# Performance work log

Measured on AMD Instinct MI355X. Metric: run time of the kernel, lower is better.

The kernel has to match this reference:

```python
import jax, jax.numpy as jnp
import numpy as np

H = 32          # hidden_size
L = 10          # linear_size
EPS = 1e-14


def _lstm_cell(x, h, c, Wih, Whh, bih, bhh):
    # torch LSTMCell: gates ordered [i, f, g, o]
    gates = x @ Wih.T + bih + h @ Whh.T + bhh
    i, f, g, o = jnp.split(gates, 4, axis=-1)
    i = jax.nn.sigmoid(i)
    f = jax.nn.sigmoid(f)
    g = jnp.tanh(g)
    o = jax.nn.sigmoid(o)
    c_new = f * c + i * g
    h_new = o * jnp.tanh(c_new)
    return h_new, c_new


def setup_inputs() -> dict:
    key = jax.random.key(0)
    ks = jax.random.split(key, 24)
    B, N = 8, 100000
    inp = {
        "x": jax.random.normal(ks[0], (B, N), jnp.float32),
        "grad": jax.random.normal(ks[1], (B, N), jnp.float32),
        "h0": jax.random.normal(ks[2], (B, N, H), jnp.float32),
        "c0": jax.random.normal(ks[3], (B, N, H), jnp.float32),
        "h1": jax.random.normal(ks[4], (B, N, H), jnp.float32),
        "c1": jax.random.normal(ks[5], (B, N, H), jnp.float32),
        # initial_transform: Linear(2, L) -> tanh -> Linear(L, L)
        "W1": jax.random.normal(ks[6], (L, 2), jnp.float32) * 0.3,
        "b1": jax.random.normal(ks[7], (L,), jnp.float32) * 0.1,
        "W2": jax.random.normal(ks[8], (L, L), jnp.float32) * 0.3,
        "b2": jax.random.normal(ks[9], (L,), jnp.float32) * 0.1,
        # LSTMCell layer 0 (input L) and layer 1 (input H)
        "Wih0": jax.random.normal(ks[10], (4 * H, L), jnp.float32) * 0.1,
        "Whh0": jax.random.normal(ks[11], (4 * H, H), jnp.float32) * 0.1,
        "bih0": jax.random.normal(ks[12], (4 * H,), jnp.float32) * 0.1,
        "bhh0": jax.random.normal(ks[13], (4 * H,), jnp.float32) * 0.1,
        "Wih1": jax.random.normal(ks[14], (4 * H, H), jnp.float32) * 0.1,
        "Whh1": jax.random.normal(ks[15], (4 * H, H), jnp.float32) * 0.1,
        "bih1": jax.random.normal(ks[16], (4 * H,), jnp.float32) * 0.1,
        "bhh1": jax.random.normal(ks[17], (4 * H,), jnp.float32) * 0.1,
        # fc: Linear(H, 1)
        "Wfc": jax.random.normal(ks[18], (1, H), jnp.float32) * 0.1,
        "bfc": jax.random.normal(ks[19], (1,), jnp.float32) * 0.1,
    }
    return inp


def reference(x, grad, h0, c0, h1, c1, W1, b1, W2, b2,
              Wih0, Whh0, bih0, bhh0, Wih1, Whh1, bih1, bhh1, Wfc, bfc):
    B, N = x.shape
    BN = B * N
    g = grad.reshape(BN, 1)
    # gradient preprocessing: [sign, log(|g| + eps)]
    inp = jnp.concatenate([jnp.sign(g), jnp.log(jnp.abs(g) + EPS)], axis=1)  # (BN, 2)
    t = jnp.tanh(inp @ W1.T + b1) @ W2.T + b2                                # (BN, L)
    # batched across all n variables simultaneously (no cross-variable recurrence)
    h0n, c0n = _lstm_cell(t, h0.reshape(BN, H), c0.reshape(BN, H), Wih0, Whh0, bih0, bhh0)
    h1n, c1n = _lstm_cell(h0n, h1.reshape(BN, H), c1.reshape(BN, H), Wih1, Whh1, bih1, bhh1)
    delta = (h1n @ Wfc.T + bfc).reshape(B, N)
    x_new = x + delta
    return (x_new,
            h0n.reshape(B, N, H), c0n.reshape(B, N, H),
            h1n.reshape(B, N, H), c1n.reshape(B, N, H),
            delta)
```

## Files before the change

kernel.cpp:

```cpp
#include <hip/hip_runtime.h>


typedef __attribute__((ext_vector_type(8))) short bf16x8;
typedef __attribute__((ext_vector_type(4))) float f32x4;

#define HH 32
#define LL 10
#define NG 128
#define NW 8
#define BLK 512

__device__ __forceinline__ short f2bf(float x) {
  __bf16 b = (__bf16)x;
  return __builtin_bit_cast(short, b);
}
__device__ __forceinline__ float fsig(float x) {
  return __builtin_amdgcn_rcpf(1.0f + __expf(-x));
}
__device__ __forceinline__ float ftanh(float x) {
  return fmaf(2.0f, __builtin_amdgcn_rcpf(1.0f + __expf(-2.0f * x)), -1.0f);
}

__global__ __launch_bounds__(BLK, 2) void l2o_fused(
    const float* __restrict__ x, const float* __restrict__ grad,
    const float* __restrict__ h0, const float* __restrict__ c0,
    const float* __restrict__ h1, const float* __restrict__ c1,
    const float* __restrict__ W1, const float* __restrict__ b1,
    const float* __restrict__ W2, const float* __restrict__ b2,
    const float* __restrict__ Wih0, const float* __restrict__ Whh0,
    const float* __restrict__ bih0, const float* __restrict__ bhh0,
    const float* __restrict__ Wih1, const float* __restrict__ Whh1,
    const float* __restrict__ bih1, const float* __restrict__ bhh1,
    const float* __restrict__ Wfc, const float* __restrict__ bfc,
    float* __restrict__ out, int BNi)
{
  const size_t BN = (size_t)BNi;
  float* __restrict__ xout  = out;
  float* __restrict__ h0out = out + BN;
  float* __restrict__ c0out = out + BN + BN * HH;
  float* __restrict__ h1out = out + BN + 2 * BN * HH;
  float* __restrict__ c1out = out + BN + 3 * BN * HH;
  float* __restrict__ dout  = out + BN + 4 * BN * HH;

  __shared__ __align__(16) short wih0L[2][NG][8];
  __shared__ __align__(16) short whh0L[4][NG][8];
  __shared__ __align__(16) short wih1L[4][NG][8];
  __shared__ __align__(16) short whh1L[4][NG][8];
  __shared__ __align__(16) short tsg0[NW][64][8];
  __shared__ __align__(4)  short tsg1[NW][64][2];
  __shared__ __align__(16) short hsg[NW][4][16][8];

  const int tid = threadIdx.x;
  for (int idx = tid; idx < NG * HH; idx += BLK) {
    int n = idx >> 5, k = idx & 31;
    whh0L[k >> 3][n][k & 7] = f2bf(Whh0[n * HH + k]);
    wih1L[k >> 3][n][k & 7] = f2bf(Wih1[n * HH + k]);
    whh1L[k >> 3][n][k & 7] = f2bf(Whh1[n * HH + k]);
  }
  for (int idx = tid; idx < NG * 16; idx += BLK) {
    int n = idx >> 4, k = idx & 15;
    wih0L[k >> 3][n][k & 7] = (k < LL) ? f2bf(Wih0[n * LL + k]) : (short)0;
  }

  const int lane = tid & 63;
  const int w = tid >> 6;
  const int col = lane & 15;
  const int g = lane >> 4;
  const int mrow = 4 * g;

  float biasv0[8], biasv1[8];
#pragma unroll
  for (int nt = 0; nt < 8; ++nt) {
    biasv0[nt] = bih0[nt * 16 + col] + bhh0[nt * 16 + col];
    biasv1[nt] = bih1[nt * 16 + col] + bhh1[nt * 16 + col];
  }
  const float wfc0 = Wfc[col], wfc1 = Wfc[16 + col];
  const float bfcv = bfc[0];

  const int ebase = blockIdx.x * (NW * 64) + w * 64;
  const bool active = ebase < BNi;

  if (active) {
    float gv = grad[ebase + lane];
    float sg = (gv > 0.f) ? 1.f : ((gv < 0.f) ? -1.f : 0.f);
    float lg = __logf(fabsf(gv) + 1e-14f);
    float u[LL], t[LL];
#pragma unroll
    for (int j = 0; j < LL; ++j)
      u[j] = ftanh(W1[2 * j] * sg + W1[2 * j + 1] * lg + b1[j]);
#pragma unroll
    for (int j = 0; j < LL; ++j) {
      float a = b2[j];
#pragma unroll
      for (int k = 0; k < LL; ++k) a += W2[j * LL + k] * u[k];
      t[j] = a;
    }
    bf16x8 tv0;
#pragma unroll
    for (int s = 0; s < 8; ++s) tv0[s] = f2bf(t[s]);
    *reinterpret_cast<bf16x8*>(&tsg0[w][lane][0]) = tv0;
    tsg1[w][lane][0] = f2bf(t[8]);
    tsg1[w][lane][1] = f2bf(t[9]);
  }
  __syncthreads();

  if (active) {
#pragma unroll 1
  for (int st = 0; st < 4; ++st) {
    const int m16 = ebase + st * 16;

    bf16x8 a_t = {0, 0, 0, 0, 0, 0, 0, 0};
    if (g == 0) a_t = *reinterpret_cast<const bf16x8*>(&tsg0[w][st * 16 + col][0]);
    else if (g == 1) {
      a_t[0] = tsg1[w][st * 16 + col][0];
      a_t[1] = tsg1[w][st * 16 + col][1];
    }
    const float4* hp = reinterpret_cast<const float4*>(h0 + (size_t)(m16 + col) * HH + 8 * g);
    float4 v0 = hp[0], v1 = hp[1];
    bf16x8 a_h0;
    a_h0[0] = f2bf(v0.x); a_h0[1] = f2bf(v0.y); a_h0[2] = f2bf(v0.z); a_h0[3] = f2bf(v0.w);
    a_h0[4] = f2bf(v1.x); a_h0[5] = f2bf(v1.y); a_h0[6] = f2bf(v1.z); a_h0[7] = f2bf(v1.w);

    float c0r[2][4];
#pragma unroll
    for (int kk = 0; kk < 2; ++kk)
#pragma unroll
      for (int r = 0; r < 4; ++r)
        c0r[kk][r] = c0[(size_t)(m16 + mrow + r) * HH + kk * 16 + col];

    f32x4 acc[8];
#pragma unroll
    for (int nt = 0; nt < 8; ++nt) {
      float bv = biasv0[nt];
      f32x4 a = {bv, bv, bv, bv};
      acc[nt] = a;
    }
#pragma unroll
    for (int nt = 0; nt < 8; ++nt) {
      bf16x8 bih = {0, 0, 0, 0, 0, 0, 0, 0};
      if (g < 2) bih = *reinterpret_cast<const bf16x8*>(&wih0L[g][nt * 16 + col][0]);
      acc[nt] = __builtin_amdgcn_mfma_f32_16x16x32_bf16(a_t, bih, acc[nt], 0, 0, 0);
      bf16x8 bhh = *reinterpret_cast<const bf16x8*>(&whh0L[g][nt * 16 + col][0]);
      acc[nt] = __builtin_amdgcn_mfma_f32_16x16x32_bf16(a_h0, bhh, acc[nt], 0, 0, 0);
    }

    const float4* h1p = reinterpret_cast<const float4*>(h1 + (size_t)(m16 + col) * HH + 8 * g);
    float4 w0 = h1p[0], w1v = h1p[1];

#pragma unroll
    for (int kk = 0; kk < 2; ++kk) {
      const int k = kk * 16 + col;
#pragma unroll
      for (int r = 0; r < 4; ++r) {
        const size_t e2 = (size_t)(m16 + mrow + r);
        float iv = fsig(acc[0 + kk][r]);
        float fv = fsig(acc[2 + kk][r]);
        float gv = ftanh(acc[4 + kk][r]);
        float ov = fsig(acc[6 + kk][r]);
        float cn = fv * c0r[kk][r] + iv * gv;
        float hn = ov * ftanh(cn);
        c0out[e2 * HH + k] = cn;
        h0out[e2 * HH + k] = hn;
        hsg[w][k >> 3][mrow + r][k & 7] = f2bf(hn);
      }
    }
    asm volatile("s_waitcnt lgkmcnt(0)" ::: "memory");

    bf16x8 a_hn = *reinterpret_cast<const bf16x8*>(&hsg[w][g][col][0]);
    bf16x8 a_h1;
    a_h1[0] = f2bf(w0.x);  a_h1[1] = f2bf(w0.y);  a_h1[2] = f2bf(w0.z);  a_h1[3] = f2bf(w0.w);
    a_h1[4] = f2bf(w1v.x); a_h1[5] = f2bf(w1v.y); a_h1[6] = f2bf(w1v.z); a_h1[7] = f2bf(w1v.w);

    float c1r[2][4];
#pragma unroll
    for (int kk = 0; kk < 2; ++kk)
#pragma unroll
      for (int r = 0; r < 4; ++r)
        c1r[kk][r] = c1[(size_t)(m16 + mrow + r) * HH + kk * 16 + col];

#pragma unroll
    for (int nt = 0; nt < 8; ++nt) {
      float bv = biasv1[nt];
      f32x4 a = {bv, bv, bv, bv};
      acc[nt] = a;
    }
#pragma unroll
    for (int nt = 0; nt < 8; ++nt) {
      bf16x8 bih = *reinterpret_cast<const bf16x8*>(&wih1L[g][nt * 16 + col][0]);
      acc[nt] = __builtin_amdgcn_mfma_f32_16x16x32_bf16(a_hn, bih, acc[nt], 0, 0, 0);
      bf16x8 bhh = *reinterpret_cast<const bf16x8*>(&whh1L[g][nt * 16 + col][0]);
      acc[nt] = __builtin_amdgcn_mfma_f32_16x16x32_bf16(a_h1, bhh, acc[nt], 0, 0, 0);
    }

    float dsum[4] = {0.f, 0.f, 0.f, 0.f};
#pragma unroll
    for (int kk = 0; kk < 2; ++kk) {
      const int k = kk * 16 + col;
      const float wf = kk ? wfc1 : wfc0;
#pragma unroll
      for (int r = 0; r < 4; ++r) {
        const size_t e2 = (size_t)(m16 + mrow + r);
        float iv = fsig(acc[0 + kk][r]);
        float fv = fsig(acc[2 + kk][r]);
        float gv = ftanh(acc[4 + kk][r]);
        float ov = fsig(acc[6 + kk][r]);
        float cn = fv * c1r[kk][r] + iv * gv;
        float hn = ov * ftanh(cn);
        c1out[e2 * HH + k] = cn;
        h1out[e2 * HH + k] = hn;
        dsum[r] += hn * wf;
      }
    }
#pragma unroll
    for (int off = 1; off < 16; off <<= 1) {
#pragma unroll
      for (int r = 0; r < 4; ++r) dsum[r] += __shfl_xor(dsum[r], off, 64);
    }
    if (col == 0) {
      const int e4 = m16 + mrow;
      float4 xv = *reinterpret_cast<const float4*>(x + e4);
      float4 dv = {dsum[0] + bfcv, dsum[1] + bfcv, dsum[2] + bfcv, dsum[3] + bfcv};
      *reinterpret_cast<float4*>(dout + e4) = dv;
      float4 xn = {xv.x + dv.x, xv.y + dv.y, xv.z + dv.z, xv.w + dv.w};
      *reinterpret_cast<float4*>(xout + e4) = xn;
    }
  }
  }
}

extern "C" void kernel_launch(void* const* d_in, const int* in_sizes, int n_in,
                              void* d_out, int out_size, void* d_ws, size_t ws_size,
                              hipStream_t stream) {
  const float* x    = (const float*)d_in[0];
  const float* grad = (const float*)d_in[1];
  const float* h0   = (const float*)d_in[2];
  const float* c0   = (const float*)d_in[3];
  const float* h1   = (const float*)d_in[4];
  const float* c1   = (const float*)d_in[5];
  const float* W1   = (const float*)d_in[6];
  const float* b1   = (const float*)d_in[7];
  const float* W2   = (const float*)d_in[8];
  const float* b2   = (const float*)d_in[9];
  const float* Wih0 = (const float*)d_in[10];
  const float* Whh0 = (const float*)d_in[11];
  const float* bih0 = (const float*)d_in[12];
  const float* bhh0 = (const float*)d_in[13];
  const float* Wih1 = (const float*)d_in[14];
  const float* Whh1 = (const float*)d_in[15];
  const float* bih1 = (const float*)d_in[16];
  const float* bhh1 = (const float*)d_in[17];
  const float* Wfc  = (const float*)d_in[18];
  const float* bfc  = (const float*)d_in[19];
  const int BN = in_sizes[0];
  const int nblk = (BN + BLK - 1) / BLK;
  l2o_fused<<<nblk, BLK, 0, stream>>>(x, grad, h0, c0, h1, c1, W1, b1, W2, b2,
                                      Wih0, Whh0, bih0, bhh0, Wih1, Whh1,
                                      bih1, bhh1, Wfc, bfc, (float*)d_out, BN);
}
```

Before: 218.5 us.

## Transpose state tiles through LDS for vectorized coalesced loads and stores

```diff
diff --git a/kernel.cpp b/kernel.cpp
--- a/kernel.cpp
+++ b/kernel.cpp
@@ -9,6 +9,7 @@
 #define NG 128
 #define NW 8
 #define BLK 512
+#define TP 36
 
 __device__ __forceinline__ short f2bf(float x) {
   __bf16 b = (__bf16)x;
@@ -20,6 +21,7 @@
 __device__ __forceinline__ float ftanh(float x) {
   return fmaf(2.0f, __builtin_amdgcn_rcpf(1.0f + __expf(-2.0f * x)), -1.0f);
 }
+#define LDS_FENCE() asm volatile("s_waitcnt lgkmcnt(0)" ::: "memory")
 
 __global__ __launch_bounds__(BLK, 2) void l2o_fused(
     const float* __restrict__ x, const float* __restrict__ grad,
@@ -48,7 +50,7 @@
   __shared__ __align__(16) short whh1L[4][NG][8];
   __shared__ __align__(16) short tsg0[NW][64][8];
   __shared__ __align__(4)  short tsg1[NW][64][2];
-  __shared__ __align__(16) short hsg[NW][4][16][8];
+  __shared__ __align__(16) float tbuf[NW][16][TP];
 
   const int tid = threadIdx.x;
   for (int idx = tid; idx < NG * HH; idx += BLK) {
@@ -108,6 +110,16 @@
 #pragma unroll 1
   for (int st = 0; st < 4; ++st) {
     const int m16 = ebase + st * 16;
+    const size_t rowoff = (size_t)(m16 + col) * HH + 8 * g;
+
+    const float4* h0p = reinterpret_cast<const float4*>(h0 + rowoff);
+    float4 hv0 = h0p[0], hv1 = h0p[1];
+    const float4* c0p = reinterpret_cast<const float4*>(c0 + rowoff);
+    float4 cv0 = c0p[0], cv1 = c0p[1];
+    const float4* h1p = reinterpret_cast<const float4*>(h1 + rowoff);
+    float4 wv0 = h1p[0], wv1 = h1p[1];
+    const float4* c1p = reinterpret_cast<const float4*>(c1 + rowoff);
+    float4 dv0 = c1p[0], dv1 = c1p[1];
 
     bf16x8 a_t = {0, 0, 0, 0, 0, 0, 0, 0};
     if (g == 0) a_t = *reinterpret_cast<const bf16x8*>(&tsg0[w][st * 16 + col][0]);
@@ -115,18 +127,9 @@
       a_t[0] = tsg1[w][st * 16 + col][0];
       a_t[1] = tsg1[w][st * 16 + col][1];
     }
-    const float4* hp = reinterpret_cast<const float4*>(h0 + (size_t)(m16 + col) * HH + 8 * g);
-    float4 v0 = hp[0], v1 = hp[1];
     bf16x8 a_h0;
-    a_h0[0] = f2bf(v0.x); a_h0[1] = f2bf(v0.y); a_h0[2] = f2bf(v0.z); a_h0[3] = f2bf(v0.w);
-    a_h0[4] = f2bf(v1.x); a_h0[5] = f2bf(v1.y); a_h0[6] = f2bf(v1.z); a_h0[7] = f2bf(v1.w);
-
-    float c0r[2][4];
-#pragma unroll
-    for (int kk = 0; kk < 2; ++kk)
-#pragma unroll
-      for (int r = 0; r < 4; ++r)
-        c0r[kk][r] = c0[(size_t)(m16 + mrow + r) * HH + kk * 16 + col];
+    a_h0[0] = f2bf(hv0.x); a_h0[1] = f2bf(hv0.y); a_h0[2] = f2bf(hv0.z); a_h0[3] = f2bf(hv0.w);
+    a_h0[4] = f2bf(hv1.x); a_h0[5] = f2bf(hv1.y); a_h0[6] = f2bf(hv1.z); a_h0[7] = f2bf(hv1.w);
 
     f32x4 acc[8];
 #pragma unroll
@@ -144,40 +147,73 @@
       acc[nt] = __builtin_amdgcn_mfma_f32_16x16x32_bf16(a_h0, bhh, acc[nt], 0, 0, 0);
     }
 
-    const float4* h1p = reinterpret_cast<const float4*>(h1 + (size_t)(m16 + col) * HH + 8 * g);
-    float4 w0 = h1p[0], w1v = h1p[1];
-
-#pragma unroll
-    for (int kk = 0; kk < 2; ++kk) {
-      const int k = kk * 16 + col;
+    *reinterpret_cast<float4*>(&tbuf[w][col][8 * g])     = cv0;
+    *reinterpret_cast<float4*>(&tbuf[w][col][8 * g + 4]) = cv1;
+    LDS_FENCE();
+    float c0r[2][4];
+#pragma unroll
+    for (int kk = 0; kk < 2; ++kk)
+#pragma unroll
+      for (int r = 0; r < 4; ++r)
+        c0r[kk][r] = tbuf[w][mrow + r][16 * kk + col];
+    LDS_FENCE();
+
+    float hnv[2][4], cnv[2][4];
+#pragma unroll
+    for (int kk = 0; kk < 2; ++kk)
 #pragma unroll
       for (int r = 0; r < 4; ++r) {
-        const size_t e2 = (size_t)(m16 + mrow + r);
         float iv = fsig(acc[0 + kk][r]);
         float fv = fsig(acc[2 + kk][r]);
         float gv = ftanh(acc[4 + kk][r]);
         float ov = fsig(acc[6 + kk][r]);
         float cn = fv * c0r[kk][r] + iv * gv;
         float hn = ov * ftanh(cn);
-        c0out[e2 * HH + k] = cn;
-        h0out[e2 * HH + k] = hn;
-        hsg[w][k >> 3][mrow + r][k & 7] = f2bf(hn);
+        cnv[kk][r] = cn;
+        hnv[kk][r] = hn;
       }
-    }
-    asm volatile("s_waitcnt lgkmcnt(0)" ::: "memory");
-
-    bf16x8 a_hn = *reinterpret_cast<const bf16x8*>(&hsg[w][g][col][0]);
+
+#pragma unroll
+    for (int kk = 0; kk < 2; ++kk)
+#pragma unroll
+      for (int r = 0; r < 4; ++r)
+        tbuf[w][mrow + r][16 * kk + col] = hnv[kk][r];
+    LDS_FENCE();
+    float4 hnr0 = *reinterpret_cast<const float4*>(&tbuf[w][col][8 * g]);
+    float4 hnr1 = *reinterpret_cast<const float4*>(&tbuf[w][col][8 * g + 4]);
+    LDS_FENCE();
+    *reinterpret_cast<float4*>(h0out + rowoff)     = hnr0;
+    *reinterpret_cast<float4*>(h0out + rowoff + 4) = hnr1;
+    bf16x8 a_hn;
+    a_hn[0] = f2bf(hnr0.x); a_hn[1] = f2bf(hnr0.y); a_hn[2] = f2bf(hnr0.z); a_hn[3] = f2bf(hnr0.w);
+    a_hn[4] = f2bf(hnr1.x); a_hn[5] = f2bf(hnr1.y); a_hn[6] = f2bf(hnr1.z); a_hn[7] = f2bf(hnr1.w);
+
+#pragma unroll
+    for (int kk = 0; kk < 2; ++kk)
+#pragma unroll
+      for (int r = 0; r < 4; ++r)
+        tbuf[w][mrow + r][16 * kk + col] = cnv[kk][r];
+    LDS_FENCE();
+    float4 cnr0 = *reinterpret_cast<const float4*>(&tbuf[w][col][8 * g]);
+    float4 cnr1 = *reinterpret_cast<const float4*>(&tbuf[w][col][8 * g + 4]);
+    LDS_FENCE();
+    *reinterpret_cast<float4*>(c0out + rowoff)     = cnr0;
+    *reinterpret_cast<float4*>(c0out + rowoff + 4) = cnr1;
+
+    *reinterpret_cast<float4*>(&tbuf[w][col][8 * g])     = dv0;
+    *reinterpret_cast<float4*>(&tbuf[w][col][8 * g + 4]) = dv1;
+    LDS_FENCE();
+    float c1r[2][4];
+#pragma unroll
+    for (int kk = 0; kk < 2; ++kk)
+#pragma unroll
+      for (int r = 0; r < 4; ++r)
+        c1r[kk][r] = tbuf[w][mrow + r][16 * kk + col];
+    LDS_FENCE();
+
     bf16x8 a_h1;
-    a_h1[0] = f2bf(w0.x);  a_h1[1] = f2bf(w0.y);  a_h1[2] = f2bf(w0.z);  a_h1[3] = f2bf(w0.w);
-    a_h1[4] = f2bf(w1v.x); a_h1[5] = f2bf(w1v.y); a_h1[6] = f2bf(w1v.z); a_h1[7] = f2bf(w1v.w);
-
-    float c1r[2][4];
-#pragma unroll
-    for (int kk = 0; kk < 2; ++kk)
-#pragma unroll
-      for (int r = 0; r < 4; ++r)
-        c1r[kk][r] = c1[(size_t)(m16 + mrow + r) * HH + kk * 16 + col];
-
+    a_h1[0] = f2bf(wv0.x); a_h1[1] = f2bf(wv0.y); a_h1[2] = f2bf(wv0.z); a_h1[3] = f2bf(wv0.w);
+    a_h1[4] = f2bf(wv1.x); a_h1[5] = f2bf(wv1.y); a_h1[6] = f2bf(wv1.z); a_h1[7] = f2bf(wv1.w);
 #pragma unroll
     for (int nt = 0; nt < 8; ++nt) {
       float bv = biasv1[nt];
@@ -195,22 +231,45 @@
     float dsum[4] = {0.f, 0.f, 0.f, 0.f};
 #pragma unroll
     for (int kk = 0; kk < 2; ++kk) {
-      const int k = kk * 16 + col;
       const float wf = kk ? wfc1 : wfc0;
 #pragma unroll
       for (int r = 0; r < 4; ++r) {
-        const size_t e2 = (size_t)(m16 + mrow + r);
         float iv = fsig(acc[0 + kk][r]);
         float fv = fsig(acc[2 + kk][r]);
         float gv = ftanh(acc[4 + kk][r]);
         float ov = fsig(acc[6 + kk][r]);
         float cn = fv * c1r[kk][r] + iv * gv;
         float hn = ov * ftanh(cn);
-        c1out[e2 * HH + k] = cn;
-        h1out[e2 * HH + k] = hn;
+        cnv[kk][r] = cn;
+        hnv[kk][r] = hn;
         dsum[r] += hn * wf;
       }
     }
+
+#pragma unroll
+    for (int kk = 0; kk < 2; ++kk)
+#pragma unroll
+      for (int r = 0; r < 4; ++r)
+        tbuf[w][mrow + r][16 * kk + col] = hnv[kk][r];
+    LDS_FENCE();
+    float4 h1r0 = *reinterpret_cast<const float4*>(&tbuf[w][col][8 * g]);
+    float4 h1r1 = *reinterpret_cast<const float4*>(&tbuf[w][col][8 * g + 4]);
+    LDS_FENCE();
+    *reinterpret_cast<float4*>(h1out + rowoff)     = h1r0;
+    *reinterpret_cast<float4*>(h1out + rowoff + 4) = h1r1;
+
+#pragma unroll
+    for (int kk = 0; kk < 2; ++kk)
+#pragma unroll
+      for (int r = 0; r < 4; ++r)
+        tbuf[w][mrow + r][16 * kk + col] = cnv[kk][r];
+    LDS_FENCE();
+    float4 c1r0 = *reinterpret_cast<const float4*>(&tbuf[w][col][8 * g]);
+    float4 c1r1 = *reinterpret_cast<const float4*>(&tbuf[w][col][8 * g + 4]);
+    LDS_FENCE();
+    *reinterpret_cast<float4*>(c1out + rowoff)     = c1r0;
+    *reinterpret_cast<float4*>(c1out + rowoff + 4) = c1r1;
+
 #pragma unroll
     for (int off = 1; off < 16; off <<= 1) {
 #pragma unroll
```

Result: faster. 209.0 us (-4.3%).

## Software-pipeline row loads and coalesce state I/O through LDS transposes

Applied to the files above, without the earlier changes.

```diff
diff --git a/kernel.cpp b/kernel.cpp
--- a/kernel.cpp
+++ b/kernel.cpp
@@ -9,6 +9,7 @@
 #define NG 128
 #define NW 8
 #define BLK 512
+#define TP 36
 
 __device__ __forceinline__ short f2bf(float x) {
   __bf16 b = (__bf16)x;
@@ -20,6 +21,181 @@
 __device__ __forceinline__ float ftanh(float x) {
   return fmaf(2.0f, __builtin_amdgcn_rcpf(1.0f + __expf(-2.0f * x)), -1.0f);
 }
+#define LDS_FENCE() asm volatile("s_waitcnt lgkmcnt(0)" ::: "memory")
+
+#define LOADT(P, STV) do {                                                   \
+    const size_t ro_ = (size_t)(ebase + (STV) * 16 + col) * HH + 8 * g;      \
+    P##hv0 = reinterpret_cast<const float4*>(h0 + ro_)[0];                   \
+    P##hv1 = reinterpret_cast<const float4*>(h0 + ro_)[1];                   \
+    P##cv0 = reinterpret_cast<const float4*>(c0 + ro_)[0];                   \
+    P##cv1 = reinterpret_cast<const float4*>(c0 + ro_)[1];                   \
+    P##wv0 = reinterpret_cast<const float4*>(h1 + ro_)[0];                   \
+    P##wv1 = reinterpret_cast<const float4*>(h1 + ro_)[1];                   \
+    P##dv0 = reinterpret_cast<const float4*>(c1 + ro_)[0];                   \
+    P##dv1 = reinterpret_cast<const float4*>(c1 + ro_)[1];                   \
+  } while (0)
+
+#define COMPUTE(P, STV) do {                                                  \
+    const int m16_ = ebase + (STV) * 16;                                      \
+    const size_t rowoff_ = (size_t)(m16_ + col) * HH + 8 * g;                 \
+    bf16x8 a_t = {0, 0, 0, 0, 0, 0, 0, 0};                                    \
+    if (g == 0) a_t = *reinterpret_cast<const bf16x8*>(&tsg0[w][(STV) * 16 + col][0]); \
+    else if (g == 1) {                                                        \
+      a_t[0] = tsg1[w][(STV) * 16 + col][0];                                  \
+      a_t[1] = tsg1[w][(STV) * 16 + col][1];                                  \
+    }                                                                         \
+    bf16x8 a_h0;                                                              \
+    a_h0[0] = f2bf(P##hv0.x); a_h0[1] = f2bf(P##hv0.y);                       \
+    a_h0[2] = f2bf(P##hv0.z); a_h0[3] = f2bf(P##hv0.w);                       \
+    a_h0[4] = f2bf(P##hv1.x); a_h0[5] = f2bf(P##hv1.y);                       \
+    a_h0[6] = f2bf(P##hv1.z); a_h0[7] = f2bf(P##hv1.w);                       \
+    f32x4 acc[8];                                                             \
+    _Pragma("unroll")                                                         \
+    for (int nt = 0; nt < 8; ++nt) {                                          \
+      float bv = biasv0[nt];                                                  \
+      f32x4 a = {bv, bv, bv, bv};                                             \
+      acc[nt] = a;                                                            \
+    }                                                                         \
+    _Pragma("unroll")                                                         \
+    for (int nt = 0; nt < 8; ++nt) {                                          \
+      bf16x8 bih = {0, 0, 0, 0, 0, 0, 0, 0};                                  \
+      if (g < 2) bih = *reinterpret_cast<const bf16x8*>(&wih0L[g][nt * 16 + col][0]); \
+      acc[nt] = __builtin_amdgcn_mfma_f32_16x16x32_bf16(a_t, bih, acc[nt], 0, 0, 0);  \
+      bf16x8 bhh = *reinterpret_cast<const bf16x8*>(&whh0L[g][nt * 16 + col][0]);     \
+      acc[nt] = __builtin_amdgcn_mfma_f32_16x16x32_bf16(a_h0, bhh, acc[nt], 0, 0, 0); \
+    }                                                                         \
+    *reinterpret_cast<float4*>(&tbuf[w][col][8 * g])     = P##cv0;            \
+    *reinterpret_cast<float4*>(&tbuf[w][col][8 * g + 4]) = P##cv1;            \
+    LDS_FENCE();                                                              \
+    float c0r[2][4];                                                          \
+    _Pragma("unroll")                                                         \
+    for (int kk = 0; kk < 2; ++kk)                                            \
+      _Pragma("unroll")                                                       \
+      for (int r = 0; r < 4; ++r)                                             \
+        c0r[kk][r] = tbuf[w][mrow + r][16 * kk + col];                        \
+    LDS_FENCE();                                                              \
+    float hnv[2][4], cnv[2][4];                                               \
+    _Pragma("unroll")                                                         \
+    for (int kk = 0; kk < 2; ++kk)                                            \
+      _Pragma("unroll")                                                       \
+      for (int r = 0; r < 4; ++r) {                                           \
+        float iv = fsig(acc[0 + kk][r]);                                      \
+        float fv = fsig(acc[2 + kk][r]);                                      \
+        float gv = ftanh(acc[4 + kk][r]);                                     \
+        float ov = fsig(acc[6 + kk][r]);                                      \
+        float cn = fv * c0r[kk][r] + iv * gv;                                 \
+        float hn = ov * ftanh(cn);                                            \
+        cnv[kk][r] = cn;                                                      \
+        hnv[kk][r] = hn;                                                      \
+      }                                                                       \
+    _Pragma("unroll")                                                         \
+    for (int kk = 0; kk < 2; ++kk)                                            \
+      _Pragma("unroll")                                                       \
+      for (int r = 0; r < 4; ++r)                                             \
+        tbuf[w][mrow + r][16 * kk + col] = hnv[kk][r];                        \
+    LDS_FENCE();                                                              \
+    float4 hnr0 = *reinterpret_cast<const float4*>(&tbuf[w][col][8 * g]);     \
+    float4 hnr1 = *reinterpret_cast<const float4*>(&tbuf[w][col][8 * g + 4]); \
+    LDS_FENCE();                                                              \
+    *reinterpret_cast<float4*>(h0out + rowoff_)     = hnr0;                   \
+    *reinterpret_cast<float4*>(h0out + rowoff_ + 4) = hnr1;                   \
+    bf16x8 a_hn;                                                              \
+    a_hn[0] = f2bf(hnr0.x); a_hn[1] = f2bf(hnr0.y);                           \
+    a_hn[2] = f2bf(hnr0.z); a_hn[3] = f2bf(hnr0.w);                           \
+    a_hn[4] = f2bf(hnr1.x); a_hn[5] = f2bf(hnr1.y);                           \
+    a_hn[6] = f2bf(hnr1.z); a_hn[7] = f2bf(hnr1.w);                           \
+    _Pragma("unroll")                                                         \
+    for (int kk = 0; kk < 2; ++kk)                                            \
+      _Pragma("unroll")                                                       \
+      for (int r = 0; r < 4; ++r)                                             \
+        tbuf[w][mrow + r][16 * kk + col] = cnv[kk][r];                        \
+    LDS_FENCE();                                                              \
+    float4 cnr0 = *reinterpret_cast<const float4*>(&tbuf[w][col][8 * g]);     \
+    float4 cnr1 = *reinterpret_cast<const float4*>(&tbuf[w][col][8 * g + 4]); \
+    LDS_FENCE();                                                              \
+    *reinterpret_cast<float4*>(c0out + rowoff_)     = cnr0;                   \
+    *reinterpret_cast<float4*>(c0out + rowoff_ + 4) = cnr1;                   \
+    *reinterpret_cast<float4*>(&tbuf[w][col][8 * g])     = P##dv0;            \
+    *reinterpret_cast<float4*>(&tbuf[w][col][8 * g + 4]) = P##dv1;            \
+    LDS_FENCE();                                                              \
+    float c1r[2][4];                                                          \
+    _Pragma("unroll")                                                         \
+    for (int kk = 0; kk < 2; ++kk)                                            \
+      _Pragma("unroll")                                                       \
+      for (int r = 0; r < 4; ++r)                                             \
+        c1r[kk][r] = tbuf[w][mrow + r][16 * kk + col];                        \
+    LDS_FENCE();                                                              \
+    bf16x8 a_h1;                                                              \
+    a_h1[0] = f2bf(P##wv0.x); a_h1[1] = f2bf(P##wv0.y);                       \
+    a_h1[2] = f2bf(P##wv0.z); a_h1[3] = f2bf(P##wv0.w);                       \
+    a_h1[4] = f2bf(P##wv1.x); a_h1[5] = f2bf(P##wv1.y);                       \
+    a_h1[6] = f2bf(P##wv1.z); a_h1[7] = f2bf(P##wv1.w);                       \
+    _Pragma("unroll")                                                         \
+    for (int nt = 0; nt < 8; ++nt) {                                          \
+      float bv = biasv1[nt];                                                  \
+      f32x4 a = {bv, bv, bv, bv};                                             \
+      acc[nt] = a;                                                            \
+    }                                                                         \
+    _Pragma("unroll")                                                         \
+    for (int nt = 0; nt < 8; ++nt) {                                          \
+      bf16x8 bih = *reinterpret_cast<const bf16x8*>(&wih1L[g][nt * 16 + col][0]);     \
+      acc[nt] = __builtin_amdgcn_mfma_f32_16x16x32_bf16(a_hn, bih, acc[nt], 0, 0, 0); \
+      bf16x8 bhh = *reinterpret_cast<const bf16x8*>(&whh1L[g][nt * 16 + col][0]);     \
+      acc[nt] = __builtin_amdgcn_mfma_f32_16x16x32_bf16(a_h1, bhh, acc[nt], 0, 0, 0); \
+    }                                                                         \
+    float dsum[4] = {0.f, 0.f, 0.f, 0.f};                                     \
+    _Pragma("unroll")                                                         \
+    for (int kk = 0; kk < 2; ++kk) {                                          \
+      const float wf = kk ? wfc1 : wfc0;                                      \
+      _Pragma("unroll")                                                       \
+      for (int r = 0; r < 4; ++r) {                                           \
+        float iv = fsig(acc[0 + kk][r]);                                      \
+        float fv = fsig(acc[2 + kk][r]);                                      \
+        float gv = ftanh(acc[4 + kk][r]);                                     \
+        float ov = fsig(acc[6 + kk][r]);                                      \
+        float cn = fv * c1r[kk][r] + iv * gv;                                 \
+        float hn = ov * ftanh(cn);                                            \
+        cnv[kk][r] = cn;                                                      \
+        hnv[kk][r] = hn;                                                      \
+        dsum[r] += hn * wf;                                                   \
+      }                                                                       \
+    }                                                                         \
+    _Pragma("unroll")                                                         \
+    for (int kk = 0; kk < 2; ++kk)                                            \
+      _Pragma("unroll")                                                       \
+      for (int r = 0; r < 4; ++r)                                             \
+        tbuf[w][mrow + r][16 * kk + col] = hnv[kk][r];                        \
+    LDS_FENCE();                                                              \
+    float4 h1r0 = *reinterpret_cast<const float4*>(&tbuf[w][col][8 * g]);     \
+    float4 h1r1 = *reinterpret_cast<const float4*>(&tbuf[w][col][8 * g + 4]); \
+    LDS_FENCE();                                                              \
+    *reinterpret_cast<float4*>(h1out + rowoff_)     = h1r0;                   \
+    *reinterpret_cast<float4*>(h1out + rowoff_ + 4) = h1r1;                   \
+    _Pragma("unroll")                                                         \
+    for (int kk = 0; kk < 2; ++kk)                                            \
+      _Pragma("unroll")                                                       \
+      for (int r = 0; r < 4; ++r)                                             \
+        tbuf[w][mrow + r][16 * kk + col] = cnv[kk][r];                        \
+    LDS_FENCE();                                                              \
+    float4 c1r0 = *reinterpret_cast<const float4*>(&tbuf[w][col][8 * g]);     \
+    float4 c1r1 = *reinterpret_cast<const float4*>(&tbuf[w][col][8 * g + 4]); \
+    LDS_FENCE();                                                              \
+    *reinterpret_cast<float4*>(c1out + rowoff_)     = c1r0;                   \
+    *reinterpret_cast<float4*>(c1out + rowoff_ + 4) = c1r1;                   \
+    _Pragma("unroll")                                                         \
+    for (int off = 1; off < 16; off <<= 1) {                                  \
+      _Pragma("unroll")                                                       \
+      for (int r = 0; r < 4; ++r) dsum[r] += __shfl_xor(dsum[r], off, 64);    \
+    }                                                                         \
+    if (col == 0) {                                                           \
+      const int e4 = m16_ + mrow;                                             \
+      float4 xv = *reinterpret_cast<const float4*>(x + e4);                   \
+      float4 dv = {dsum[0] + bfcv, dsum[1] + bfcv, dsum[2] + bfcv, dsum[3] + bfcv}; \
+      *reinterpret_cast<float4*>(dout + e4) = dv;                             \
+      float4 xn = {xv.x + dv.x, xv.y + dv.y, xv.z + dv.z, xv.w + dv.w};       \
+      *reinterpret_cast<float4*>(xout + e4) = xn;                             \
+    }                                                                         \
+  } while (0)
 
 __global__ __launch_bounds__(BLK, 2) void l2o_fused(
     const float* __restrict__ x, const float* __restrict__ grad,
@@ -48,9 +224,23 @@
   __shared__ __align__(16) short whh1L[4][NG][8];
   __shared__ __align__(16) short tsg0[NW][64][8];
   __shared__ __align__(4)  short tsg1[NW][64][2];
-  __shared__ __align__(16) short hsg[NW][4][16][8];
+  __shared__ __align__(16) float tbuf[NW][16][TP];
 
   const int tid = threadIdx.x;
+  const int lane = tid & 63;
+  const int w = tid >> 6;
+  const int col = lane & 15;
+  const int g = lane >> 4;
+  const int mrow = 4 * g;
+
+  const int ebase = blockIdx.x * (NW * 64) + w * 64;
+  const bool active = ebase < BNi;
+
+  float4 Ahv0, Ahv1, Acv0, Acv1, Awv0, Awv1, Adv0, Adv1;
+  float4 Bhv0, Bhv1, Bcv0, Bcv1, Bwv0, Bwv1, Bdv0, Bdv1;
+
+  if (active) LOADT(A, 0);
+
   for (int idx = tid; idx < NG * HH; idx += BLK) {
     int n = idx >> 5, k = idx & 31;
     whh0L[k >> 3][n][k & 7] = f2bf(Whh0[n * HH + k]);
@@ -62,12 +252,6 @@
     wih0L[k >> 3][n][k & 7] = (k < LL) ? f2bf(Wih0[n * LL + k]) : (short)0;
   }
 
-  const int lane = tid & 63;
-  const int w = tid >> 6;
-  const int col = lane & 15;
-  const int g = lane >> 4;
-  const int mrow = 4 * g;
-
   float biasv0[8], biasv1[8];
 #pragma unroll
   for (int nt = 0; nt < 8; ++nt) {
@@ -76,9 +260,6 @@
   }
   const float wfc0 = Wfc[col], wfc1 = Wfc[16 + col];
   const float bfcv = bfc[0];
-
-  const int ebase = blockIdx.x * (NW * 64) + w * 64;
-  const bool active = ebase < BNi;
 
   if (active) {
     float gv = grad[ebase + lane];
@@ -105,126 +286,13 @@
   __syncthreads();
 
   if (active) {
-#pragma unroll 1
-  for (int st = 0; st < 4; ++st) {
-    const int m16 = ebase + st * 16;
-
-    bf16x8 a_t = {0, 0, 0, 0, 0, 0, 0, 0};
-    if (g == 0) a_t = *reinterpret_cast<const bf16x8*>(&tsg0[w][st * 16 + col][0]);
-    else if (g == 1) {
-      a_t[0] = tsg1[w][st * 16 + col][0];
-      a_t[1] = tsg1[w][st * 16 + col][1];
-    }
-    const float4* hp = reinterpret_cast<const float4*>(h0 + (size_t)(m16 + col) * HH + 8 * g);
-    float4 v0 = hp[0], v1 = hp[1];
-    bf16x8 a_h0;
-    a_h0[0] = f2bf(v0.x); a_h0[1] = f2bf(v0.y); a_h0[2] = f2bf(v0.z); a_h0[3] = f2bf(v0.w);
-    a_h0[4] = f2bf(v1.x); a_h0[5] = f2bf(v1.y); a_h0[6] = f2bf(v1.z); a_h0[7] = f2bf(v1.w);
-
-    float c0r[2][4];
-#pragma unroll
-    for (int kk = 0; kk < 2; ++kk)
-#pragma unroll
-      for (int r = 0; r < 4; ++r)
-        c0r[kk][r] = c0[(size_t)(m16 + mrow + r) * HH + kk * 16 + col];
-
-    f32x4 acc[8];
-#pragma unroll
-    for (int nt = 0; nt < 8; ++nt) {
-      float bv = biasv0[nt];
-      f32x4 a = {bv, bv, bv, bv};
-      acc[nt] = a;
-    }
-#pragma unroll
-    for (int nt = 0; nt < 8; ++nt) {
-      bf16x8 bih = {0, 0, 0, 0, 0, 0, 0, 0};
-      if (g < 2) bih = *reinterpret_cast<const bf16x8*>(&wih0L[g][nt * 16 + col][0]);
-      acc[nt] = __builtin_amdgcn_mfma_f32_16x16x32_bf16(a_t, bih, acc[nt], 0, 0, 0);
-      bf16x8 bhh = *reinterpret_cast<const bf16x8*>(&whh0L[g][nt * 16 + col][0]);
-      acc[nt] = __builtin_amdgcn_mfma_f32_16x16x32_bf16(a_h0, bhh, acc[nt], 0, 0, 0);
-    }
-
-    const float4* h1p = reinterpret_cast<const float4*>(h1 + (size_t)(m16 + col) * HH + 8 * g);
-    float4 w0 = h1p[0], w1v = h1p[1];
-
-#pragma unroll
-    for (int kk = 0; kk < 2; ++kk) {
-      const int k = kk * 16 + col;
-#pragma unroll
-      for (int r = 0; r < 4; ++r) {
-        const size_t e2 = (size_t)(m16 + mrow + r);
-        float iv = fsig(acc[0 + kk][r]);
-        float fv = fsig(acc[2 + kk][r]);
-        float gv = ftanh(acc[4 + kk][r]);
-        float ov = fsig(acc[6 + kk][r]);
-        float cn = fv * c0r[kk][r] + iv * gv;
-        float hn = ov * ftanh(cn);
-        c0out[e2 * HH + k] = cn;
-        h0out[e2 * HH + k] = hn;
-        hsg[w][k >> 3][mrow + r][k & 7] = f2bf(hn);
-      }
-    }
-    asm volatile("s_waitcnt lgkmcnt(0)" ::: "memory");
-
-    bf16x8 a_hn = *reinterpret_cast<const bf16x8*>(&hsg[w][g][col][0]);
-    bf16x8 a_h1;
-    a_h1[0] = f2bf(w0.x);  a_h1[1] = f2bf(w0.y);  a_h1[2] = f2bf(w0.z);  a_h1[3] = f2bf(w0.w);
-    a_h1[4] = f2bf(w1v.x); a_h1[5] = f2bf(w1v.y); a_h1[6] = f2bf(w1v.z); a_h1[7] = f2bf(w1v.w);
-
-    float c1r[2][4];
-#pragma unroll
-    for (int kk = 0; kk < 2; ++kk)
-#pragma unroll
-      for (int r = 0; r < 4; ++r)
-        c1r[kk][r] = c1[(size_t)(m16 + mrow + r) * HH + kk * 16 + col];
-
-#pragma unroll
-    for (int nt = 0; nt < 8; ++nt) {
-      float bv = biasv1[nt];
-      f32x4 a = {bv, bv, bv, bv};
-      acc[nt] = a;
-    }
-#pragma unroll
-    for (int nt = 0; nt < 8; ++nt) {
-      bf16x8 bih = *reinterpret_cast<const bf16x8*>(&wih1L[g][nt * 16 + col][0]);
-      acc[nt] = __builtin_amdgcn_mfma_f32_16x16x32_bf16(a_hn, bih, acc[nt], 0, 0, 0);
-      bf16x8 bhh = *reinterpret_cast<const bf16x8*>(&whh1L[g][nt * 16 + col][0]);
-      acc[nt] = __builtin_amdgcn_mfma_f32_16x16x32_bf16(a_h1, bhh, acc[nt], 0, 0, 0);
-    }
-
-    float dsum[4] = {0.f, 0.f, 0.f, 0.f};
-#pragma unroll
-    for (int kk = 0; kk < 2; ++kk) {
-      const int k = kk * 16 + col;
-      const float wf = kk ? wfc1 : wfc0;
-#pragma unroll
-      for (int r = 0; r < 4; ++r) {
-        const size_t e2 = (size_t)(m16 + mrow + r);
-        float iv = fsig(acc[0 + kk][r]);
-        float fv = fsig(acc[2 + kk][r]);
-        float gv = ftanh(acc[4 + kk][r]);
-        float ov = fsig(acc[6 + kk][r]);
-        float cn = fv * c1r[kk][r] + iv * gv;
-        float hn = ov * ftanh(cn);
-        c1out[e2 * HH + k] = cn;
-        h1out[e2 * HH + k] = hn;
-        dsum[r] += hn * wf;
-      }
-    }
-#pragma unroll
-    for (int off = 1; off < 16; off <<= 1) {
-#pragma unroll
-      for (int r = 0; r < 4; ++r) dsum[r] += __shfl_xor(dsum[r], off, 64);
-    }
-    if (col == 0) {
-      const int e4 = m16 + mrow;
-      float4 xv = *reinterpret_cast<const float4*>(x + e4);
-      float4 dv = {dsum[0] + bfcv, dsum[1] + bfcv, dsum[2] + bfcv, dsum[3] + bfcv};
-      *reinterpret_cast<float4*>(dout + e4) = dv;
-      float4 xn = {xv.x + dv.x, xv.y + dv.y, xv.z + dv.z, xv.w + dv.w};
-      *reinterpret_cast<float4*>(xout + e4) = xn;
-    }
-  }
+    LOADT(B, 1);
+    COMPUTE(A, 0);
+    LOADT(A, 2);
+    COMPUTE(B, 1);
+    LOADT(B, 3);
+    COMPUTE(A, 2);
+    COMPUTE(B, 3);
   }
 }
 
```

After: 208.8 us. 1.05x faster.
